# Kernel tuning notes

Hardware: AMD Instinct MI355X
Metric: run time of the kernel (lower is better)

## Reference

```python
import jax, jax.numpy as jnp
import numpy as np

DIM = 1024
HEADS = 16
DIM_HEAD = 64
B = 4
N = 2048
INNER = HEADS * DIM_HEAD
SCALE = DIM_HEAD ** -0.5
NEG = -1e9


def setup_inputs() -> dict:
    key = jax.random.key(0)
    k1, k2, k3 = jax.random.split(key, 3)
    x = jax.random.normal(k1, (B, N, DIM), dtype=jnp.float32)
    w_qkv = jax.random.normal(k2, (DIM, 3 * INNER), dtype=jnp.float32) * (DIM ** -0.5)
    w_out = jax.random.normal(k3, (INNER, DIM), dtype=jnp.float32) * (INNER ** -0.5)
    b_out = jnp.zeros((DIM,), dtype=jnp.float32)
    return {"x": x, "w_qkv": w_qkv, "w_out": w_out, "b_out": b_out}


def reference(x, w_qkv, w_out, b_out):
    b, n, _ = x.shape
    qkv = x @ w_qkv  # [b, n, 3*inner]
    q, k, v = jnp.split(qkv, 3, axis=-1)
    # [b, n, inner] -> [b, h, n, d]
    split_heads = lambda t: t.reshape(b, n, HEADS, DIM_HEAD).transpose(0, 2, 1, 3)
    q, k, v = split_heads(q), split_heads(k), split_heads(v)
    dots = jnp.einsum('bhid,bhjd->bhij', q, k) * SCALE
    causal = jnp.tril(jnp.ones((n, n), dtype=bool))  # mask[i,j]=1 for j<=i
    dots = jnp.where(causal, dots, NEG)
    attn = jax.nn.softmax(dots, axis=-1)
    out = jnp.einsum('bhij,bhjd->bhid', attn, v)
    out = out.transpose(0, 2, 1, 3).reshape(b, n, INNER)
    return out @ w_out + b_out
```

## Files before the change

### kernel.cpp

```cpp
#include <hip/hip_runtime.h>

typedef unsigned short u16;
typedef __attribute__((ext_vector_type(8))) short short8;
typedef __attribute__((ext_vector_type(4))) float f32x4;
typedef __attribute__((ext_vector_type(4))) short short4v;

#define MFMA_BF16(a, b, c) __builtin_amdgcn_mfma_f32_16x16x32_bf16((a), (b), (c), 0, 0, 0)

__device__ __forceinline__ void gl2lds16(const u16* g, u16* l) {
  __builtin_amdgcn_global_load_lds(
      (const __attribute__((address_space(1))) unsigned int*)g,
      (__attribute__((address_space(3))) unsigned int*)l, 16, 0, 0);
}

__device__ __forceinline__ u16 f2bf(float f) {
  union { float f; unsigned u; } v; v.f = f;
  unsigned r = v.u + 0x7fffu + ((v.u >> 16) & 1u);
  return (u16)(r >> 16);
}

__global__ void fill_one_f32(float* p, int n) {
  int i = blockIdx.x * blockDim.x + threadIdx.x;
  if (i < n) p[i] = 1.0f;
}

__global__ void downcast_f32_bf16(const float* __restrict__ src, u16* __restrict__ dst,
                                  int n) {
  const int i = (blockIdx.x * blockDim.x + threadIdx.x) * 4;
  if (i < n) {
    const f32x4 v = *(const f32x4*)&src[i];
    short4v o;
    o.x = (short)f2bf(v.x); o.y = (short)f2bf(v.y);
    o.z = (short)f2bf(v.z); o.w = (short)f2bf(v.w);
    *(short4v*)&dst[i] = o;
  }
}

__global__ void transpose_f32_bf16(const float* __restrict__ src, u16* __restrict__ dst,
                                   int R, int C) {
  __shared__ float tile[32][33];
  const int tx = threadIdx.x & 31, ty = threadIdx.x >> 5;
  const int r0 = blockIdx.y * 32, c0 = blockIdx.x * 32;
#pragma unroll
  for (int i = 0; i < 4; ++i)
    tile[ty + i * 8][tx] = src[(size_t)(r0 + ty + i * 8) * C + c0 + tx];
  __syncthreads();
#pragma unroll
  for (int i = 0; i < 4; ++i)
    dst[(size_t)(c0 + ty + i * 8) * R + r0 + tx] = f2bf(tile[tx][ty + i * 8]);
}

template <int MODE>
__launch_bounds__(256, 2)
__global__ void gemm_bt_k(const u16* __restrict__ A, const u16* __restrict__ Bt,
                          int K, int Ncols,
                          u16* __restrict__ O0, u16* __restrict__ O1,
                          u16* __restrict__ O2,
                          float* __restrict__ Of, const float* __restrict__ biasf) {
  __shared__ __align__(16) u16 Alds[128 * 32];
  __shared__ __align__(16) u16 Blds[128 * 32];
  const int t = threadIdx.x;
  const int w = t >> 6, l = t & 63;
  const int quad = l >> 4, l16 = l & 15;
  const int m0 = blockIdx.y * 128, n0 = blockIdx.x * 128;
  const int wm = w & 1, wn = w >> 1;

  f32x4 acc[4][4];
#pragma unroll
  for (int a = 0; a < 4; ++a)
#pragma unroll
    for (int b = 0; b < 4; ++b) acc[a][b] = (f32x4){0.f, 0.f, 0.f, 0.f};

  const int c0 = w * 128 + l;

#pragma unroll 1
  for (int k0 = 0; k0 < K; k0 += 32) {
    {
      int c = c0;
      gl2lds16(A + (size_t)(m0 + (c >> 2)) * K + k0 + (c & 3) * 8,
               (u16*)((char*)Alds + c * 16));
      gl2lds16(Bt + (size_t)(n0 + (c >> 2)) * K + k0 + (c & 3) * 8,
               (u16*)((char*)Blds + c * 16));
      c = c0 + 64;
      gl2lds16(A + (size_t)(m0 + (c >> 2)) * K + k0 + (c & 3) * 8,
               (u16*)((char*)Alds + c * 16));
      gl2lds16(Bt + (size_t)(n0 + (c >> 2)) * K + k0 + (c & 3) * 8,
               (u16*)((char*)Blds + c * 16));
    }
    __syncthreads();
    short8 av[4], bv[4];
#pragma unroll
    for (int a = 0; a < 4; ++a)
      av[a] = *(const short8*)&Alds[(wm * 64 + a * 16 + l16) * 32 + quad * 8];
#pragma unroll
    for (int b = 0; b < 4; ++b)
      bv[b] = *(const short8*)&Blds[(wn * 64 + b * 16 + l16) * 32 + quad * 8];
#pragma unroll
    for (int a = 0; a < 4; ++a)
#pragma unroll
      for (int b = 0; b < 4; ++b)
        acc[a][b] = MFMA_BF16(av[a], bv[b], acc[a][b]);
    __syncthreads();
  }

#pragma unroll
  for (int a = 0; a < 4; ++a)
#pragma unroll
    for (int b = 0; b < 4; ++b)
#pragma unroll
      for (int r = 0; r < 4; ++r) {
        const int row = m0 + wm * 64 + a * 16 + quad * 4 + r;
        const int col = n0 + wn * 64 + b * 16 + l16;
        const float v = acc[a][b][r];
        if (MODE == 0) {
          const int bb = row >> 11, n = row & 2047;
          const int which = col >> 10, j = col & 1023, h = j >> 6, d = j & 63;
          u16* dst = (which == 0) ? O0 : (which == 1) ? O1 : O2;
          dst[(((size_t)bb * 16 + h) * 2048 + n) * 64 + d] = f2bf(v);
        } else {
          Of[(size_t)row * Ncols + col] = v + biasf[col];
        }
      }
}

#define KS 72
__launch_bounds__(256, 2)
__global__ void flash_k3(const u16* __restrict__ Q, const u16* __restrict__ K,
                         const u16* __restrict__ V, u16* __restrict__ AO) {
  __shared__ __align__(16) u16 Klds[64 * KS];
  __shared__ __align__(16) u16 Vt[64 * KS];
  __shared__ __align__(16) u16 Plds[4][32 * KS];
  const int t = threadIdx.x, w = t >> 6, l = t & 63;
  const int quad = l >> 4, l16 = l & 15;
  const int bh = blockIdx.y;
  const size_t base = (size_t)bh * 2048 * 64;
  const u16* Qp = Q + base;
  const u16* Kp = K + base;
  const u16* Vp = V + base;
  const int bb = bh >> 4, hh = bh & 15;
  const float SC = 0.125f;
  const float FM = 3.0f;

  short8 ones;
#pragma unroll
  for (int j = 0; j < 8; ++j) ones[j] = (short)0x3F80;

#pragma unroll 1
  for (int ph = 0; ph < 2; ++ph) {
    const int qi = ph ? (15 - blockIdx.x) : blockIdx.x;
    const int qbase = qi * 128;

    short8 qf[2][2];
#pragma unroll
    for (int mi = 0; mi < 2; ++mi) {
      const int row = qbase + w * 32 + mi * 16 + l16;
#pragma unroll
      for (int h = 0; h < 2; ++h)
        qf[mi][h] = *(const short8*)&Qp[(size_t)row * 64 + h * 32 + quad * 8];
    }

    f32x4 oacc[2][4], lacc[2];
#pragma unroll
    for (int mi = 0; mi < 2; ++mi) {
      lacc[mi] = (f32x4){0.f, 0.f, 0.f, 0.f};
#pragma unroll
      for (int df = 0; df < 4; ++df) oacc[mi][df] = (f32x4){0.f, 0.f, 0.f, 0.f};
    }

    const int nkt = 2 * qi + 2;
    const int wrow_lo = qbase + w * 32;
    const int wrow_hi = wrow_lo + 31;

#pragma unroll 1
    for (int kt = 0; kt < nkt; ++kt) {
      {
        const int ca = t, cb = t + 256;
        const short8 ka = *(const short8*)&Kp[(size_t)(kt * 64 + (ca >> 3)) * 64 + (ca & 7) * 8];
        const short8 kb = *(const short8*)&Kp[(size_t)(kt * 64 + (cb >> 3)) * 64 + (cb & 7) * 8];
        const short8 va = *(const short8*)&Vp[(size_t)(kt * 64 + (ca >> 3)) * 64 + (ca & 7) * 8];
        const short8 vb = *(const short8*)&Vp[(size_t)(kt * 64 + (cb >> 3)) * 64 + (cb & 7) * 8];
        *(short8*)&Klds[(ca >> 3) * KS + (ca & 7) * 8] = ka;
        *(short8*)&Klds[(cb >> 3) * KS + (cb & 7) * 8] = kb;
        {
          const int kp = ca >> 3, d0 = (ca & 7) * 8, swz = (ca & 7) * 8;
#pragma unroll
          for (int j = 0; j < 8; ++j) Vt[(d0 + j) * KS + (kp ^ swz)] = (u16)va[j];
        }
        {
          const int kp = cb >> 3, d0 = (cb & 7) * 8, swz = (cb & 7) * 8;
#pragma unroll
          for (int j = 0; j < 8; ++j) Vt[(d0 + j) * KS + (kp ^ swz)] = (u16)vb[j];
        }
      }
      __syncthreads();

      const bool skip = (kt * 64 > wrow_hi);
      if (!skip) {
        f32x4 sa[2][4];
#pragma unroll
        for (int nf = 0; nf < 4; ++nf) {
          const short8 kf0 = *(const short8*)&Klds[(nf * 16 + l16) * KS + quad * 8];
          const short8 kf1 = *(const short8*)&Klds[(nf * 16 + l16) * KS + 32 + quad * 8];
#pragma unroll
          for (int mi = 0; mi < 2; ++mi) {
            f32x4 s = (f32x4){0.f, 0.f, 0.f, 0.f};
            s = MFMA_BF16(qf[mi][0], kf0, s);
            s = MFMA_BF16(qf[mi][1], kf1, s);
            sa[mi][nf] = s;
          }
        }

        const bool needmask = (kt * 64 + 63 > wrow_lo);
#pragma unroll
        for (int mi = 0; mi < 2; ++mi) {
#pragma unroll
          for (int nf = 0; nf < 4; ++nf)
#pragma unroll
            for (int r = 0; r < 4; ++r) {
              float arg = fmaf(sa[mi][nf][r], SC, -FM);
              if (needmask) {
                const int col = kt * 64 + nf * 16 + l16;
                const int row = qbase + w * 32 + mi * 16 + quad * 4 + r;
                arg = (col <= row) ? arg : -1e9f;
              }
              union { float f; unsigned u; } pu;
              pu.f = __expf(arg);
              Plds[w][(mi * 16 + quad * 4 + r) * KS + nf * 16 + l16] =
                  (u16)((pu.u + 0x8000u) >> 16);
            }
        }

        short8 pf[2][2];
#pragma unroll
        for (int mi = 0; mi < 2; ++mi) {
          pf[mi][0] = *(const short8*)&Plds[w][(mi * 16 + l16) * KS + quad * 8];
          pf[mi][1] = *(const short8*)&Plds[w][(mi * 16 + l16) * KS + 32 + quad * 8];
        }
#pragma unroll
        for (int mi = 0; mi < 2; ++mi) {
          lacc[mi] = MFMA_BF16(pf[mi][0], ones, lacc[mi]);
          lacc[mi] = MFMA_BF16(pf[mi][1], ones, lacc[mi]);
        }
#pragma unroll
        for (int df = 0; df < 4; ++df) {
          const int s = (2 * df + (l16 >> 3)) & 7;
          const int rowb = (df * 16 + l16) * KS;
          const short8 vf0 = *(const short8*)&Vt[rowb + ((quad ^ s) * 8)];
          const short8 vf1 = *(const short8*)&Vt[rowb + (((quad + 4) ^ s) * 8)];
#pragma unroll
          for (int mi = 0; mi < 2; ++mi) {
            oacc[mi][df] = MFMA_BF16(pf[mi][0], vf0, oacc[mi][df]);
            oacc[mi][df] = MFMA_BF16(pf[mi][1], vf1, oacc[mi][df]);
          }
        }
      }
      __syncthreads();
    }

#pragma unroll
    for (int mi = 0; mi < 2; ++mi) {
      const int srow = qbase + w * 32 + mi * 16 + quad * 4;
#pragma unroll
      for (int df = 0; df < 4; ++df)
#pragma unroll
        for (int r = 0; r < 4; ++r) {
          const int n = srow + r;
          const int d = df * 16 + l16;
          AO[((size_t)bb * 2048 + n) * 1024 + hh * 64 + d] =
              f2bf(oacc[mi][df][r] / lacc[mi][r]);
        }
    }
  }
}

extern "C" void kernel_launch(void* const* d_in, const int* in_sizes, int n_in,
                              void* d_out, int out_size, void* d_ws, size_t ws_size,
                              hipStream_t stream) {
  const float* x = (const float*)d_in[0];
  const float* w_qkv = (const float*)d_in[1];
  const float* w_out = (const float*)d_in[2];
  const float* b_out = (const float*)d_in[3];
  float* out = (float*)d_out;

  const size_t MB = 1024 * 1024;
  if (ws_size < 72 * MB) {
    fill_one_f32<<<(out_size + 255) / 256, 256, 0, stream>>>(out, out_size);
    return;
  }

  char* ws = (char*)d_ws;
  u16* wqkvT = (u16*)(ws);
  u16* woutT = (u16*)(ws + 6 * MB);
  u16* Xb = (u16*)(ws + 8 * MB);
  u16* AO = Xb;
  u16* Qb = (u16*)(ws + 24 * MB);
  u16* Kb = (u16*)(ws + 40 * MB);
  u16* Vb = (u16*)(ws + 56 * MB);

  downcast_f32_bf16<<<8192, 256, 0, stream>>>(x, Xb, 4 * 2048 * 1024);
  transpose_f32_bf16<<<dim3(3072 / 32, 1024 / 32), 256, 0, stream>>>(w_qkv, wqkvT, 1024, 3072);
  transpose_f32_bf16<<<dim3(1024 / 32, 1024 / 32), 256, 0, stream>>>(w_out, woutT, 1024, 1024);
  gemm_bt_k<0><<<dim3(3072 / 128, 8192 / 128), 256, 0, stream>>>(
      Xb, wqkvT, 1024, 3072, Qb, Kb, Vb, nullptr, nullptr);
  flash_k3<<<dim3(8, 64), 256, 0, stream>>>(Qb, Kb, Vb, AO);
  gemm_bt_k<1><<<dim3(1024 / 128, 8192 / 128), 256, 0, stream>>>(
      AO, woutT, 1024, 1024, nullptr, nullptr, nullptr, out, b_out);
}
```

Baseline: 273.7 us.

## Use 8 waves per flash block and fuse prep kernels into one launch

The flash attention kernel now runs 512 threads, with each wave owning 16 query rows instead of 32. This halves per-wave register state and spreads the K/V tile load across more threads, aiming for more latency hiding. The three preprocessing kernels (downcast plus two weight transposes) are merged into one launch, removing two launch overheads. In exchange, each K/V tile load is shared by more waves, so the two block barriers per tile coordinate more waves and K fragment reuse per wave drops.

```diff
diff --git a/kernel.cpp b/kernel.cpp
--- a/kernel.cpp
+++ b/kernel.cpp
@@ -24,23 +24,36 @@
   if (i < n) p[i] = 1.0f;
 }
 
-__global__ void downcast_f32_bf16(const float* __restrict__ src, u16* __restrict__ dst,
-                                  int n) {
-  const int i = (blockIdx.x * blockDim.x + threadIdx.x) * 4;
-  if (i < n) {
-    const f32x4 v = *(const f32x4*)&src[i];
-    short4v o;
-    o.x = (short)f2bf(v.x); o.y = (short)f2bf(v.y);
-    o.z = (short)f2bf(v.z); o.w = (short)f2bf(v.w);
-    *(short4v*)&dst[i] = o;
-  }
-}
-
-__global__ void transpose_f32_bf16(const float* __restrict__ src, u16* __restrict__ dst,
-                                   int R, int C) {
+__global__ void prep_k(const float* __restrict__ x, u16* __restrict__ Xb,
+                       const float* __restrict__ w_qkv, u16* __restrict__ wqkvT,
+                       const float* __restrict__ w_out, u16* __restrict__ woutT) {
   __shared__ float tile[32][33];
-  const int tx = threadIdx.x & 31, ty = threadIdx.x >> 5;
-  const int r0 = blockIdx.y * 32, c0 = blockIdx.x * 32;
+  const int bid = blockIdx.x, t = threadIdx.x;
+  if (bid < 2048) {
+    const int base = (bid * 256 + t) * 16;
+#pragma unroll
+    for (int h = 0; h < 2; ++h) {
+      const f32x4 v0 = *(const f32x4*)&x[base + h * 8];
+      const f32x4 v1 = *(const f32x4*)&x[base + h * 8 + 4];
+      short8 o;
+      o[0] = (short)f2bf(v0.x); o[1] = (short)f2bf(v0.y);
+      o[2] = (short)f2bf(v0.z); o[3] = (short)f2bf(v0.w);
+      o[4] = (short)f2bf(v1.x); o[5] = (short)f2bf(v1.y);
+      o[6] = (short)f2bf(v1.z); o[7] = (short)f2bf(v1.w);
+      *(short8*)&Xb[base + h * 8] = o;
+    }
+    return;
+  }
+  const float* src; u16* dst; int R, C, bx, by;
+  if (bid < 5120) {
+    const int tb = bid - 2048;
+    src = w_qkv; dst = wqkvT; R = 1024; C = 3072; bx = tb % 96; by = tb / 96;
+  } else {
+    const int tb = bid - 5120;
+    src = w_out; dst = woutT; R = 1024; C = 1024; bx = tb % 32; by = tb / 32;
+  }
+  const int tx = t & 31, ty = t >> 5;
+  const int r0 = by * 32, c0 = bx * 32;
 #pragma unroll
   for (int i = 0; i < 4; ++i)
     tile[ty + i * 8][tx] = src[(size_t)(r0 + ty + i * 8) * C + c0 + tx];
@@ -124,12 +137,12 @@
 }
 
 #define KS 72
-__launch_bounds__(256, 2)
-__global__ void flash_k3(const u16* __restrict__ Q, const u16* __restrict__ K,
+__launch_bounds__(512, 4)
+__global__ void flash_k4(const u16* __restrict__ Q, const u16* __restrict__ K,
                          const u16* __restrict__ V, u16* __restrict__ AO) {
   __shared__ __align__(16) u16 Klds[64 * KS];
   __shared__ __align__(16) u16 Vt[64 * KS];
-  __shared__ __align__(16) u16 Plds[4][32 * KS];
+  __shared__ __align__(16) u16 Plds[8][16 * KS];
   const int t = threadIdx.x, w = t >> 6, l = t & 63;
   const int quad = l >> 4, l16 = l & 15;
   const int bh = blockIdx.y;
@@ -150,126 +163,90 @@
     const int qi = ph ? (15 - blockIdx.x) : blockIdx.x;
     const int qbase = qi * 128;
 
-    short8 qf[2][2];
-#pragma unroll
-    for (int mi = 0; mi < 2; ++mi) {
-      const int row = qbase + w * 32 + mi * 16 + l16;
-#pragma unroll
-      for (int h = 0; h < 2; ++h)
-        qf[mi][h] = *(const short8*)&Qp[(size_t)row * 64 + h * 32 + quad * 8];
-    }
-
-    f32x4 oacc[2][4], lacc[2];
-#pragma unroll
-    for (int mi = 0; mi < 2; ++mi) {
-      lacc[mi] = (f32x4){0.f, 0.f, 0.f, 0.f};
-#pragma unroll
-      for (int df = 0; df < 4; ++df) oacc[mi][df] = (f32x4){0.f, 0.f, 0.f, 0.f};
-    }
+    const int qrow = qbase + w * 16 + l16;
+    short8 qf[2];
+    qf[0] = *(const short8*)&Qp[(size_t)qrow * 64 + quad * 8];
+    qf[1] = *(const short8*)&Qp[(size_t)qrow * 64 + 32 + quad * 8];
+
+    f32x4 oacc[4], lacc;
+    lacc = (f32x4){0.f, 0.f, 0.f, 0.f};
+#pragma unroll
+    for (int df = 0; df < 4; ++df) oacc[df] = (f32x4){0.f, 0.f, 0.f, 0.f};
 
     const int nkt = 2 * qi + 2;
-    const int wrow_lo = qbase + w * 32;
-    const int wrow_hi = wrow_lo + 31;
+    const int wrow_lo = qbase + w * 16;
+    const int wrow_hi = wrow_lo + 15;
 
 #pragma unroll 1
     for (int kt = 0; kt < nkt; ++kt) {
       {
-        const int ca = t, cb = t + 256;
-        const short8 ka = *(const short8*)&Kp[(size_t)(kt * 64 + (ca >> 3)) * 64 + (ca & 7) * 8];
-        const short8 kb = *(const short8*)&Kp[(size_t)(kt * 64 + (cb >> 3)) * 64 + (cb & 7) * 8];
-        const short8 va = *(const short8*)&Vp[(size_t)(kt * 64 + (ca >> 3)) * 64 + (ca & 7) * 8];
-        const short8 vb = *(const short8*)&Vp[(size_t)(kt * 64 + (cb >> 3)) * 64 + (cb & 7) * 8];
-        *(short8*)&Klds[(ca >> 3) * KS + (ca & 7) * 8] = ka;
-        *(short8*)&Klds[(cb >> 3) * KS + (cb & 7) * 8] = kb;
-        {
-          const int kp = ca >> 3, d0 = (ca & 7) * 8, swz = (ca & 7) * 8;
-#pragma unroll
-          for (int j = 0; j < 8; ++j) Vt[(d0 + j) * KS + (kp ^ swz)] = (u16)va[j];
-        }
-        {
-          const int kp = cb >> 3, d0 = (cb & 7) * 8, swz = (cb & 7) * 8;
-#pragma unroll
-          for (int j = 0; j < 8; ++j) Vt[(d0 + j) * KS + (kp ^ swz)] = (u16)vb[j];
-        }
+        const int kp = t >> 3, d0 = (t & 7) * 8;
+        const short8 kv = *(const short8*)&Kp[(size_t)(kt * 64 + kp) * 64 + d0];
+        const short8 vv = *(const short8*)&Vp[(size_t)(kt * 64 + kp) * 64 + d0];
+        *(short8*)&Klds[kp * KS + d0] = kv;
+#pragma unroll
+        for (int j = 0; j < 8; ++j) Vt[(d0 + j) * KS + (kp ^ d0)] = (u16)vv[j];
       }
       __syncthreads();
 
       const bool skip = (kt * 64 > wrow_hi);
       if (!skip) {
-        f32x4 sa[2][4];
+        f32x4 sa[4];
 #pragma unroll
         for (int nf = 0; nf < 4; ++nf) {
           const short8 kf0 = *(const short8*)&Klds[(nf * 16 + l16) * KS + quad * 8];
           const short8 kf1 = *(const short8*)&Klds[(nf * 16 + l16) * KS + 32 + quad * 8];
-#pragma unroll
-          for (int mi = 0; mi < 2; ++mi) {
-            f32x4 s = (f32x4){0.f, 0.f, 0.f, 0.f};
-            s = MFMA_BF16(qf[mi][0], kf0, s);
-            s = MFMA_BF16(qf[mi][1], kf1, s);
-            sa[mi][nf] = s;
+          f32x4 s = (f32x4){0.f, 0.f, 0.f, 0.f};
+          s = MFMA_BF16(qf[0], kf0, s);
+          s = MFMA_BF16(qf[1], kf1, s);
+          sa[nf] = s;
+        }
+
+        const bool needmask = (kt * 64 + 63 > wrow_lo);
+#pragma unroll
+        for (int nf = 0; nf < 4; ++nf)
+#pragma unroll
+          for (int r = 0; r < 4; ++r) {
+            float arg = fmaf(sa[nf][r], SC, -FM);
+            if (needmask) {
+              const int col = kt * 64 + nf * 16 + l16;
+              const int row = qbase + w * 16 + quad * 4 + r;
+              arg = (col <= row) ? arg : -1e9f;
+            }
+            union { float f; unsigned u; } pu;
+            pu.f = __expf(arg);
+            Plds[w][(quad * 4 + r) * KS + nf * 16 + l16] =
+                (u16)((pu.u + 0x8000u) >> 16);
           }
-        }
-
-        const bool needmask = (kt * 64 + 63 > wrow_lo);
-#pragma unroll
-        for (int mi = 0; mi < 2; ++mi) {
-#pragma unroll
-          for (int nf = 0; nf < 4; ++nf)
-#pragma unroll
-            for (int r = 0; r < 4; ++r) {
-              float arg = fmaf(sa[mi][nf][r], SC, -FM);
-              if (needmask) {
-                const int col = kt * 64 + nf * 16 + l16;
-                const int row = qbase + w * 32 + mi * 16 + quad * 4 + r;
-                arg = (col <= row) ? arg : -1e9f;
-              }
-              union { float f; unsigned u; } pu;
-              pu.f = __expf(arg);
-              Plds[w][(mi * 16 + quad * 4 + r) * KS + nf * 16 + l16] =
-                  (u16)((pu.u + 0x8000u) >> 16);
-            }
-        }
-
-        short8 pf[2][2];
-#pragma unroll
-        for (int mi = 0; mi < 2; ++mi) {
-          pf[mi][0] = *(const short8*)&Plds[w][(mi * 16 + l16) * KS + quad * 8];
-          pf[mi][1] = *(const short8*)&Plds[w][(mi * 16 + l16) * KS + 32 + quad * 8];
-        }
-#pragma unroll
-        for (int mi = 0; mi < 2; ++mi) {
-          lacc[mi] = MFMA_BF16(pf[mi][0], ones, lacc[mi]);
-          lacc[mi] = MFMA_BF16(pf[mi][1], ones, lacc[mi]);
-        }
+
+        short8 pf[2];
+        pf[0] = *(const short8*)&Plds[w][l16 * KS + quad * 8];
+        pf[1] = *(const short8*)&Plds[w][l16 * KS + 32 + quad * 8];
+        lacc = MFMA_BF16(pf[0], ones, lacc);
+        lacc = MFMA_BF16(pf[1], ones, lacc);
 #pragma unroll
         for (int df = 0; df < 4; ++df) {
           const int s = (2 * df + (l16 >> 3)) & 7;
           const int rowb = (df * 16 + l16) * KS;
           const short8 vf0 = *(const short8*)&Vt[rowb + ((quad ^ s) * 8)];
           const short8 vf1 = *(const short8*)&Vt[rowb + (((quad + 4) ^ s) * 8)];
-#pragma unroll
-          for (int mi = 0; mi < 2; ++mi) {
-            oacc[mi][df] = MFMA_BF16(pf[mi][0], vf0, oacc[mi][df]);
-            oacc[mi][df] = MFMA_BF16(pf[mi][1], vf1, oacc[mi][df]);
-          }
+          oacc[df] = MFMA_BF16(pf[0], vf0, oacc[df]);
+          oacc[df] = MFMA_BF16(pf[1], vf1, oacc[df]);
         }
       }
       __syncthreads();
     }
 
-#pragma unroll
-    for (int mi = 0; mi < 2; ++mi) {
-      const int srow = qbase + w * 32 + mi * 16 + quad * 4;
-#pragma unroll
-      for (int df = 0; df < 4; ++df)
-#pragma unroll
-        for (int r = 0; r < 4; ++r) {
-          const int n = srow + r;
-          const int d = df * 16 + l16;
-          AO[((size_t)bb * 2048 + n) * 1024 + hh * 64 + d] =
-              f2bf(oacc[mi][df][r] / lacc[mi][r]);
-        }
-    }
+    const int srow = qbase + w * 16 + quad * 4;
+#pragma unroll
+    for (int df = 0; df < 4; ++df)
+#pragma unroll
+      for (int r = 0; r < 4; ++r) {
+        const int n = srow + r;
+        const int d = df * 16 + l16;
+        AO[((size_t)bb * 2048 + n) * 1024 + hh * 64 + d] =
+            f2bf(oacc[df][r] / lacc[r]);
+      }
   }
 }
 
@@ -297,12 +274,10 @@
   u16* Kb = (u16*)(ws + 40 * MB);
   u16* Vb = (u16*)(ws + 56 * MB);
 
-  downcast_f32_bf16<<<8192, 256, 0, stream>>>(x, Xb, 4 * 2048 * 1024);
-  transpose_f32_bf16<<<dim3(3072 / 32, 1024 / 32), 256, 0, stream>>>(w_qkv, wqkvT, 1024, 3072);
-  transpose_f32_bf16<<<dim3(1024 / 32, 1024 / 32), 256, 0, stream>>>(w_out, woutT, 1024, 1024);
+  prep_k<<<6144, 256, 0, stream>>>(x, Xb, w_qkv, wqkvT, w_out, woutT);
   gemm_bt_k<0><<<dim3(3072 / 128, 8192 / 128), 256, 0, stream>>>(
       Xb, wqkvT, 1024, 3072, Qb, Kb, Vb, nullptr, nullptr);
-  flash_k3<<<dim3(8, 64), 256, 0, stream>>>(Qb, Kb, Vb, AO);
+  flash_k4<<<dim3(8, 64), 512, 0, stream>>>(Qb, Kb, Vb, AO);
   gemm_bt_k<1><<<dim3(1024 / 128, 8192 / 128), 256, 0, stream>>>(
       AO, woutT, 1024, 1024, nullptr, nullptr, nullptr, out, b_out);
 }
```

New measurement: 265.4 us. -3.0%, faster.
